# Optimization experiments

Hardware: AMD Instinct MI355X
Metric: run time of the kernel (lower is better)

The kernel has to match this reference:

```python
import jax, jax.numpy as jnp
import numpy as np

STATE = 256
IN = 128
OUT = 128


def setup_inputs() -> dict:
    key = jax.random.key(0)
    ks = jax.random.split(key, 10)
    u = jax.random.normal(ks[0], (8, 2048, IN), dtype=jnp.float32)
    x0_re = jax.random.normal(ks[1], (8, STATE), dtype=jnp.float32)
    x0_im = jax.random.normal(ks[2], (8, STATE), dtype=jnp.float32)
    # A init: 2*pi*rand angles on unit circle, scaled by 10 (enforce_stability=True)
    theta = 2.0 * jnp.pi * jax.random.uniform(ks[3], (STATE,), dtype=jnp.float32)
    A_re = 10.0 * jnp.cos(theta)
    A_im = 10.0 * jnp.sin(theta)
    # complex randn: real/imag parts each have variance 1/2
    inv_sqrt2 = 1.0 / np.sqrt(2.0)
    sB = inv_sqrt2 / np.sqrt(STATE + IN)
    B_re = jax.random.normal(ks[4], (IN, STATE), dtype=jnp.float32) * sB
    B_im = jax.random.normal(ks[5], (IN, STATE), dtype=jnp.float32) * sB
    sC = inv_sqrt2 / np.sqrt(STATE + OUT)
    C_re = jax.random.normal(ks[6], (STATE, OUT), dtype=jnp.float32) * sC
    C_im = jax.random.normal(ks[7], (STATE, OUT), dtype=jnp.float32) * sC
    D = jnp.zeros((IN, OUT), dtype=jnp.float32)
    b = jnp.zeros((OUT,), dtype=jnp.float32)
    return {"u": u, "x0_re": x0_re, "x0_im": x0_im, "A_re": A_re, "A_im": A_im,
            "B_re": B_re, "B_im": B_im, "C_re": C_re, "C_im": C_im, "D": D, "b": b}


def reference(u, x0_re, x0_im, A_re, A_im, B_re, B_im, C_re, C_im, D, b):
    cdt = jnp.complex64
    length = u.shape[1]
    A = (A_re + 1j * A_im).astype(cdt)
    # enforce_stability: map poles inside unit disc
    A = A / jnp.sqrt(A * jnp.conj(A) + 1.0)
    # Vandermonde powers A^t for t in [0, length]  -> [length+1, n]
    Aps = A[None, :] ** jnp.arange(length + 1)[:, None]
    Bm = (B_re + 1j * B_im).astype(cdt)
    uB = u.astype(cdt) @ Bm  # [batch, length, n]
    # FFT-based causal convolution of Aps[:-1] ([length, n]) with uB
    T = 2 ** int(np.ceil(np.log2(2 * length - 1)))
    AF = jnp.fft.fft(Aps[:-1], n=T, axis=0)      # [T, n]
    UF = jnp.fft.fft(uB, n=T, axis=1)            # [batch, T, n]
    x = jnp.fft.ifft(AF[None] * UF, axis=1)[:, :length]  # [batch, length, n]
    # add initial-state contribution A^t * x0
    x0 = (x0_re + 1j * x0_im).astype(cdt)
    x = x + Aps[1:][None] * x0[:, None, :]
    Cm = (C_re + 1j * C_im).astype(cdt)
    y = jnp.real(x @ Cm) + u @ D + b
    return y, x[:, -1]
```

## Files before the change

kernel.cpp:

```cpp
#include <hip/hip_runtime.h>
#include <math.h>

#define BATCH 8
#define T 2048
#define N 256
#define INF 128
#define OUTF 128
#define L 16
#define LOG2L 4
#define NC (T / L)
#define KTOT 640
#define NKS 20
#define NKU 4
#define UBS 516

typedef __attribute__((ext_vector_type(8))) short short8;
typedef __attribute__((ext_vector_type(4))) float f32x4;

__device__ __forceinline__ unsigned short f2b(float f) {
    union { float f; unsigned u; } x; x.f = f;
    unsigned r = (x.u + 0x7FFFu + ((x.u >> 16) & 1u)) >> 16;
    return (unsigned short)r;
}
__device__ __forceinline__ float b2f(unsigned short s) {
    union { unsigned u; float f; } x; x.u = ((unsigned)s) << 16;
    return x.f;
}

__global__ __launch_bounds__(256) void k_prep(const float* __restrict__ Are,
                                              const float* __restrict__ Aim,
                                              const float* __restrict__ Bre,
                                              const float* __restrict__ Bim,
                                              const float* __restrict__ Cre,
                                              const float* __restrict__ Cim,
                                              const float* __restrict__ D,
                                              float2* __restrict__ Apow,
                                              unsigned short* __restrict__ Bswz,
                                              unsigned short* __restrict__ Bswz2) {
    int blk = blockIdx.x;
    int tid = threadIdx.x;
    if (blk < 40) {
        int unit = blk * 4 + (tid >> 6);
        int ks = unit >> 3, ot = unit & 7;
        int l = tid & 63;
        int o = ot * 16 + (l & 15);
        int k0 = ks * 32 + (l >> 4) * 8;
        short8 out;
#pragma unroll
        for (int j = 0; j < 8; ++j) {
            int gk = k0 + j;
            float v = (gk < 256) ? Cre[gk * OUTF + o]
                    : (gk < 512) ? -Cim[(gk - 256) * OUTF + o]
                                 : D[(gk - 512) * OUTF + o];
            out[j] = (short)f2b(v);
        }
        *(short8*)(Bswz + ((size_t)unit * 64 + l) * 8) = out;
    } else if (blk < 72) {
        int unit = (blk - 40) * 4 + (tid >> 6);
        int l = tid & 63;
        int col = (unit & 31) * 16 + (l & 15);
        int k0 = (unit >> 5) * 32 + (l >> 4) * 8;
        short8 out;
#pragma unroll
        for (int j = 0; j < 8; ++j) {
            int gk = k0 + j;
            float v = (col < 256) ? Bre[gk * N + col] : Bim[gk * N + col - 256];
            out[j] = (short)f2b(v);
        }
        *(short8*)(Bswz2 + ((size_t)unit * 64 + l) * 8) = out;
    } else {
        int n = tid;
        float ar = Are[n], ai = Aim[n];
        float inv = 1.0f / sqrtf(ar * ar + ai * ai + 1.0f);
        ar *= inv; ai *= inv;
        float pr = ar, pi = ai;
        for (int j = 0; j < L; ++j) {
            Apow[j * N + n] = make_float2(pr, pi);
            float nr = pr * ar - pi * ai;
            float ni = pr * ai + pi * ar;
            pr = nr; pi = ni;
        }
    }
}

__global__ __launch_bounds__(512, 2) void kU_scan(const float* __restrict__ u,
                                                  const unsigned short* __restrict__ Bswz2,
                                                  const float2* __restrict__ Apow,
                                                  unsigned short* __restrict__ xbb,
                                                  float2* __restrict__ carr) {
    __shared__ float uB[32][UBS];
    int tid = threadIdx.x;
    int lane = tid & 63;
    int w = tid >> 6;
    int rg = w >> 2;
    int cq = w & 3;
    size_t row0 = (size_t)blockIdx.x * 32;
    const float* uprow = u + (row0 + rg * 16 + (lane & 15)) * INF + (lane >> 4) * 8;

    f32x4 acc[8];
#pragma unroll
    for (int i = 0; i < 8; ++i) acc[i] = (f32x4){0.f, 0.f, 0.f, 0.f};

    const short8* Bfr2 = (const short8*)Bswz2;
#pragma unroll
    for (int ks = 0; ks < NKU; ++ks) {
        float4 a0 = *(const float4*)(uprow + ks * 32);
        float4 a1 = *(const float4*)(uprow + ks * 32 + 4);
        short8 af;
        af[0] = (short)f2b(a0.x); af[1] = (short)f2b(a0.y);
        af[2] = (short)f2b(a0.z); af[3] = (short)f2b(a0.w);
        af[4] = (short)f2b(a1.x); af[5] = (short)f2b(a1.y);
        af[6] = (short)f2b(a1.z); af[7] = (short)f2b(a1.w);
#pragma unroll
        for (int i = 0; i < 8; ++i) {
            int ct = cq * 8 + i;
            short8 bf = Bfr2[(size_t)(ks * 32 + ct) * 64 + lane];
            acc[i] = __builtin_amdgcn_mfma_f32_16x16x32_bf16(af, bf, acc[i], 0, 0, 0);
        }
    }
    {
        int rbase = rg * 16 + (lane >> 4) * 4;
        int cb = lane & 15;
#pragma unroll
        for (int i = 0; i < 8; ++i) {
            int col = (cq * 8 + i) * 16 + cb;
#pragma unroll
            for (int r = 0; r < 4; ++r)
                uB[rbase + r][col] = acc[i][r];
        }
    }
    __syncthreads();

    int ch = tid >> 8;
    int n = tid & 255;
    size_t rowg0 = row0 + ch * 16;
    int b = (int)(rowg0 >> 11);
    int c = (int)((rowg0 & 2047) >> LOG2L);
    float2 a = Apow[n];
    float xr = 0.f, xi = 0.f;
#pragma unroll
    for (int j = 0; j < 16; ++j) {
        float ur = uB[ch * 16 + j][n];
        float ui = uB[ch * 16 + j][256 + n];
        float nr = fmaf(a.x, xr, fmaf(-a.y, xi, ur));
        float ni = fmaf(a.x, xi, fmaf(a.y, xr, ui));
        xr = nr; xi = ni;
        size_t rowg = rowg0 + j;
        xbb[rowg * 512 + n]       = f2b(xr);
        xbb[rowg * 512 + 256 + n] = f2b(xi);
    }
    carr[((size_t)b * NC + c) * N + n] = make_float2(xr, xi);
}

__global__ __launch_bounds__(256) void k2_carry(const float* __restrict__ x0re,
                                                const float* __restrict__ x0im,
                                                const float2* __restrict__ Apow,
                                                float2* __restrict__ carr,
                                                float* __restrict__ out_tail,
                                                int tail_mode) {
    int b = blockIdx.x, n = threadIdx.x;
    float pr = x0re[b * N + n], pi = x0im[b * N + n];
    float2 aL = Apow[(L - 1) * N + n];
#pragma unroll 8
    for (int c = 0; c < NC; ++c) {
        size_t off = ((size_t)b * NC + c) * N + n;
        float2 f = carr[off];
        carr[off] = make_float2(pr, pi);
        float nr = f.x + aL.x * pr - aL.y * pi;
        float ni = f.y + aL.x * pi + aL.y * pr;
        pr = nr; pi = ni;
    }
    if (tail_mode == 2) {
        out_tail[(b * N + n) * 2 + 0] = pr;
        out_tail[(b * N + n) * 2 + 1] = pi;
    } else if (tail_mode == 1) {
        out_tail[b * N + n] = pr;
    }
}

__global__ __launch_bounds__(256) void k3_mfma(const unsigned short* __restrict__ xbb,
                                               const float2* __restrict__ Apow,
                                               const float2* __restrict__ carr,
                                               const float* __restrict__ u,
                                               const unsigned short* __restrict__ Bswz,
                                               const float* __restrict__ bias,
                                               float* __restrict__ y) {
    int tid = threadIdx.x;
    int lane = tid & 63;
    int w = tid >> 6;
    size_t rowg = (size_t)blockIdx.x * 64 + w * 16 + (lane & 15);
    int koff = (lane >> 4) * 8;
    int t = (int)(rowg & 2047);
    int b = (int)(rowg >> 11);
    int j = t & (L - 1);
    int c = t >> LOG2L;
    const float4* Ap4 = (const float4*)(Apow + (size_t)j * N);
    const float4* Cv4 = (const float4*)(carr + ((size_t)b * NC + c) * N);
    const unsigned short* arow = xbb + rowg * 512 + koff;
    const float* urow = u + rowg * INF + koff;
    const short8* Bfr = (const short8*)Bswz;

    f32x4 acc[8];
#pragma unroll
    for (int ot = 0; ot < 8; ++ot) acc[ot] = (f32x4){0.f, 0.f, 0.f, 0.f};

#pragma unroll 2
    for (int ks = 0; ks < 16; ++ks) {
        short8 xv = *(const short8*)(arow + ks * 32);
        int re = (ks < 8);
        int n0 = (ks & 7) * 32 + koff;
        float4 ap[4], vv[4];
#pragma unroll
        for (int q = 0; q < 4; ++q) {
            ap[q] = Ap4[(n0 >> 1) + q];
            vv[q] = Cv4[(n0 >> 1) + q];
        }
        short8 af;
#pragma unroll
        for (int e = 0; e < 8; ++e) {
            float4 aq = ap[e >> 1];
            float4 vq = vv[e >> 1];
            float pr = (e & 1) ? aq.z : aq.x;
            float pi = (e & 1) ? aq.w : aq.y;
            float vr = (e & 1) ? vq.z : vq.x;
            float vi = (e & 1) ? vq.w : vq.y;
            float corr = re ? (pr * vr - pi * vi) : (pr * vi + pi * vr);
            af[e] = (short)f2b(b2f((unsigned short)xv[e]) + corr);
        }
#pragma unroll
        for (int ot = 0; ot < 8; ++ot) {
            short8 bf = Bfr[((size_t)ks * 8 + ot) * 64 + lane];
            acc[ot] = __builtin_amdgcn_mfma_f32_16x16x32_bf16(af, bf, acc[ot], 0, 0, 0);
        }
    }
#pragma unroll
    for (int ks2 = 0; ks2 < 4; ++ks2) {
        float4 a0 = *(const float4*)(urow + ks2 * 32);
        float4 a1 = *(const float4*)(urow + ks2 * 32 + 4);
        short8 af;
        af[0] = (short)f2b(a0.x); af[1] = (short)f2b(a0.y);
        af[2] = (short)f2b(a0.z); af[3] = (short)f2b(a0.w);
        af[4] = (short)f2b(a1.x); af[5] = (short)f2b(a1.y);
        af[6] = (short)f2b(a1.z); af[7] = (short)f2b(a1.w);
#pragma unroll
        for (int ot = 0; ot < 8; ++ot) {
            short8 bf = Bfr[((size_t)(16 + ks2) * 8 + ot) * 64 + lane];
            acc[ot] = __builtin_amdgcn_mfma_f32_16x16x32_bf16(af, bf, acc[ot], 0, 0, 0);
        }
    }

    int colb = lane & 15;
    int rq = lane >> 4;
    size_t rowout = (size_t)blockIdx.x * 64 + w * 16 + rq * 4;
#pragma unroll
    for (int ot = 0; ot < 8; ++ot) {
        int o = ot * 16 + colb;
        float bv = bias[o];
#pragma unroll
        for (int r = 0; r < 4; ++r) {
            y[(rowout + r) * OUTF + o] = acc[ot][r] + bv;
        }
    }
}

extern "C" void kernel_launch(void* const* d_in, const int* in_sizes, int n_in,
                              void* d_out, int out_size, void* d_ws, size_t ws_size,
                              hipStream_t stream) {
    const float* u    = (const float*)d_in[0];
    const float* x0re = (const float*)d_in[1];
    const float* x0im = (const float*)d_in[2];
    const float* Are  = (const float*)d_in[3];
    const float* Aim  = (const float*)d_in[4];
    const float* Bre  = (const float*)d_in[5];
    const float* Bim  = (const float*)d_in[6];
    const float* Cre  = (const float*)d_in[7];
    const float* Cim  = (const float*)d_in[8];
    const float* D    = (const float*)d_in[9];
    const float* bias = (const float*)d_in[10];
    float* y = (float*)d_out;

    char* ws = (char*)d_ws;
    float2* Apow = (float2*)ws;
    char* p = ws + (size_t)L * N * sizeof(float2);
    float2* carr = (float2*)p;
    p += (size_t)BATCH * NC * N * sizeof(float2);
    unsigned short* xbb = (unsigned short*)p;
    p += (size_t)BATCH * T * 512 * sizeof(unsigned short);
    unsigned short* Bswz = (unsigned short*)p;
    p += (size_t)NKS * 8 * 64 * 8 * sizeof(unsigned short);
    unsigned short* Bswz2 = (unsigned short*)p;

    const int ysz = BATCH * T * OUTF;
    const int tail_elems = out_size - ysz;
    int tail_mode = (tail_elems >= BATCH * N * 2) ? 2
                  : (tail_elems >= BATCH * N) ? 1 : 0;
    float* tail = y + ysz;

    k_prep<<<73, 256, 0, stream>>>(Are, Aim, Bre, Bim, Cre, Cim, D, Apow, Bswz, Bswz2);
    kU_scan<<<(BATCH * T) / 32, 512, 0, stream>>>(u, Bswz2, Apow, xbb, carr);
    k2_carry<<<BATCH, 256, 0, stream>>>(x0re, x0im, Apow, carr, tail, tail_mode);
    k3_mfma<<<(BATCH * T) / 64, 256, 0, stream>>>(xbb, Apow, carr, u, Bswz, bias, y);
}
```

Measured before the change: 64.52 us.

## Shrink scan blocks to one chunk each and share A-power loads across real/imag

kU_scan now processes 16 rows per 512-thread block instead of 32. That halves shared memory and accumulators, doubles the grid and raises the occupancy hint, but only half the threads run the recurrence. In k3_mfma each loop iteration now handles the real and imaginary K-slices together. The A-power and carry loads and the correction products are therefore computed once per pair instead of twice, at the cost of more live registers.

```diff
diff --git a/kernel.cpp b/kernel.cpp
--- a/kernel.cpp
+++ b/kernel.cpp
@@ -83,23 +83,21 @@
     }
 }
 
-__global__ __launch_bounds__(512, 2) void kU_scan(const float* __restrict__ u,
+__global__ __launch_bounds__(512, 8) void kU_scan(const float* __restrict__ u,
                                                   const unsigned short* __restrict__ Bswz2,
                                                   const float2* __restrict__ Apow,
                                                   unsigned short* __restrict__ xbb,
                                                   float2* __restrict__ carr) {
-    __shared__ float uB[32][UBS];
+    __shared__ float uB[16][UBS];
     int tid = threadIdx.x;
     int lane = tid & 63;
     int w = tid >> 6;
-    int rg = w >> 2;
-    int cq = w & 3;
-    size_t row0 = (size_t)blockIdx.x * 32;
-    const float* uprow = u + (row0 + rg * 16 + (lane & 15)) * INF + (lane >> 4) * 8;
-
-    f32x4 acc[8];
-#pragma unroll
-    for (int i = 0; i < 8; ++i) acc[i] = (f32x4){0.f, 0.f, 0.f, 0.f};
+    size_t rowg0 = (size_t)blockIdx.x * 16;
+    const float* uprow = u + (rowg0 + (lane & 15)) * INF + (lane >> 4) * 8;
+
+    f32x4 acc[4];
+#pragma unroll
+    for (int i = 0; i < 4; ++i) acc[i] = (f32x4){0.f, 0.f, 0.f, 0.f};
 
     const short8* Bfr2 = (const short8*)Bswz2;
 #pragma unroll
@@ -112,18 +110,18 @@
         af[4] = (short)f2b(a1.x); af[5] = (short)f2b(a1.y);
         af[6] = (short)f2b(a1.z); af[7] = (short)f2b(a1.w);
 #pragma unroll
-        for (int i = 0; i < 8; ++i) {
-            int ct = cq * 8 + i;
+        for (int i = 0; i < 4; ++i) {
+            int ct = w * 4 + i;
             short8 bf = Bfr2[(size_t)(ks * 32 + ct) * 64 + lane];
             acc[i] = __builtin_amdgcn_mfma_f32_16x16x32_bf16(af, bf, acc[i], 0, 0, 0);
         }
     }
     {
-        int rbase = rg * 16 + (lane >> 4) * 4;
+        int rbase = (lane >> 4) * 4;
         int cb = lane & 15;
 #pragma unroll
-        for (int i = 0; i < 8; ++i) {
-            int col = (cq * 8 + i) * 16 + cb;
+        for (int i = 0; i < 4; ++i) {
+            int col = (w * 4 + i) * 16 + cb;
 #pragma unroll
             for (int r = 0; r < 4; ++r)
                 uB[rbase + r][col] = acc[i][r];
@@ -131,25 +129,25 @@
     }
     __syncthreads();
 
-    int ch = tid >> 8;
-    int n = tid & 255;
-    size_t rowg0 = row0 + ch * 16;
-    int b = (int)(rowg0 >> 11);
-    int c = (int)((rowg0 & 2047) >> LOG2L);
-    float2 a = Apow[n];
-    float xr = 0.f, xi = 0.f;
-#pragma unroll
-    for (int j = 0; j < 16; ++j) {
-        float ur = uB[ch * 16 + j][n];
-        float ui = uB[ch * 16 + j][256 + n];
-        float nr = fmaf(a.x, xr, fmaf(-a.y, xi, ur));
-        float ni = fmaf(a.x, xi, fmaf(a.y, xr, ui));
-        xr = nr; xi = ni;
-        size_t rowg = rowg0 + j;
-        xbb[rowg * 512 + n]       = f2b(xr);
-        xbb[rowg * 512 + 256 + n] = f2b(xi);
-    }
-    carr[((size_t)b * NC + c) * N + n] = make_float2(xr, xi);
+    if (tid < 256) {
+        int n = tid;
+        int b = (int)(rowg0 >> 11);
+        int c = (int)((rowg0 & 2047) >> LOG2L);
+        float2 a = Apow[n];
+        float xr = 0.f, xi = 0.f;
+#pragma unroll
+        for (int j = 0; j < 16; ++j) {
+            float ur = uB[j][n];
+            float ui = uB[j][256 + n];
+            float nr = fmaf(a.x, xr, fmaf(-a.y, xi, ur));
+            float ni = fmaf(a.x, xi, fmaf(a.y, xr, ui));
+            xr = nr; xi = ni;
+            size_t rowg = rowg0 + j;
+            xbb[rowg * 512 + n]       = f2b(xr);
+            xbb[rowg * 512 + 256 + n] = f2b(xi);
+        }
+        carr[((size_t)b * NC + c) * N + n] = make_float2(xr, xi);
+    }
 }
 
 __global__ __launch_bounds__(256) void k2_carry(const float* __restrict__ x0re,
@@ -205,17 +203,17 @@
     for (int ot = 0; ot < 8; ++ot) acc[ot] = (f32x4){0.f, 0.f, 0.f, 0.f};
 
 #pragma unroll 2
-    for (int ks = 0; ks < 16; ++ks) {
-        short8 xv = *(const short8*)(arow + ks * 32);
-        int re = (ks < 8);
-        int n0 = (ks & 7) * 32 + koff;
+    for (int g = 0; g < 8; ++g) {
+        short8 xre = *(const short8*)(arow + g * 32);
+        short8 xim = *(const short8*)(arow + (g + 8) * 32);
+        int n0 = g * 32 + koff;
         float4 ap[4], vv[4];
 #pragma unroll
         for (int q = 0; q < 4; ++q) {
             ap[q] = Ap4[(n0 >> 1) + q];
             vv[q] = Cv4[(n0 >> 1) + q];
         }
-        short8 af;
+        short8 afr, afi;
 #pragma unroll
         for (int e = 0; e < 8; ++e) {
             float4 aq = ap[e >> 1];
@@ -224,13 +222,18 @@
             float pi = (e & 1) ? aq.w : aq.y;
             float vr = (e & 1) ? vq.z : vq.x;
             float vi = (e & 1) ? vq.w : vq.y;
-            float corr = re ? (pr * vr - pi * vi) : (pr * vi + pi * vr);
-            af[e] = (short)f2b(b2f((unsigned short)xv[e]) + corr);
+            afr[e] = (short)f2b(b2f((unsigned short)xre[e]) + (pr * vr - pi * vi));
+            afi[e] = (short)f2b(b2f((unsigned short)xim[e]) + (pr * vi + pi * vr));
         }
 #pragma unroll
         for (int ot = 0; ot < 8; ++ot) {
-            short8 bf = Bfr[((size_t)ks * 8 + ot) * 64 + lane];
-            acc[ot] = __builtin_amdgcn_mfma_f32_16x16x32_bf16(af, bf, acc[ot], 0, 0, 0);
+            short8 bf = Bfr[((size_t)g * 8 + ot) * 64 + lane];
+            acc[ot] = __builtin_amdgcn_mfma_f32_16x16x32_bf16(afr, bf, acc[ot], 0, 0, 0);
+        }
+#pragma unroll
+        for (int ot = 0; ot < 8; ++ot) {
+            short8 bf = Bfr[((size_t)(g + 8) * 8 + ot) * 64 + lane];
+            acc[ot] = __builtin_amdgcn_mfma_f32_16x16x32_bf16(afi, bf, acc[ot], 0, 0, 0);
         }
     }
 #pragma unroll
@@ -297,7 +300,7 @@
     float* tail = y + ysz;
 
     k_prep<<<73, 256, 0, stream>>>(Are, Aim, Bre, Bim, Cre, Cim, D, Apow, Bswz, Bswz2);
-    kU_scan<<<(BATCH * T) / 32, 512, 0, stream>>>(u, Bswz2, Apow, xbb, carr);
+    kU_scan<<<BATCH * NC, 512, 0, stream>>>(u, Bswz2, Apow, xbb, carr);
     k2_carry<<<BATCH, 256, 0, stream>>>(x0re, x0im, Apow, carr, tail, tail_mode);
     k3_mfma<<<(BATCH * T) / 64, 256, 0, stream>>>(xbb, Apow, carr, u, Bswz, bias, y);
 }
```

After: 62.13 us. -3.7%, faster.
